# Performance work log

Hardware: AMD Instinct MI355X
Metric: run time of the kernel (lower is better)

The kernel has to match this reference:

```python
import jax, jax.numpy as jnp
import numpy as np

B, N, C = 8, 2048, 256
NGRP = 4          # n oscillator dims per group
RANK = 16         # A_rank
EPS = 1e-6        # solver eps
GN_EPS = 1e-5     # torch GroupNorm default eps


def setup_inputs() -> dict:
    key = jax.random.key(0)
    k0, k1, k2, k3 = jax.random.split(key, 4)
    x = jax.random.normal(k0, (B, N, C), jnp.float32)
    y = jax.random.normal(k1, (B, C, N), jnp.float32)
    sc = jax.random.uniform(k2, (B, N, N), jnp.float32)
    U = 0.01 * jax.random.normal(k3, (N, RANK), jnp.float32)
    omega_param = (1.0 / np.sqrt(2)).astype(np.float32) * jnp.ones((C // 2, 1), jnp.float32)
    gn_w = jnp.ones((C,), jnp.float32)
    gn_b = jnp.zeros((C,), jnp.float32)
    gamma = jnp.float32(1.0)
    return {"x": x, "y": y, "sc": sc, "U": U, "omega_param": omega_param,
            "gn_w": gn_w, "gn_b": gn_b, "gamma": gamma, "Q": 8}


def _map_to_sphere(x):
    # normalize each group of NGRP channels to unit norm
    xv = x.reshape(B, N, C // NGRP, NGRP)
    n2 = jnp.clip(jnp.sum(xv * xv, axis=-1, keepdims=True), EPS, None)
    return (xv * jax.lax.rsqrt(n2)).reshape(B, N, C)


def _project_osc(v, x):
    # remove component of v along x within each oscillator group (tangent projection)
    xv = x.reshape(B, N, C // NGRP, NGRP)
    vv = v.reshape(B, N, C // NGRP, NGRP)
    sim = jnp.sum(xv * vv, axis=-1, keepdims=True)
    return (vv - sim * xv).reshape(B, N, C)


def _group_norm(y, w, b):
    # y: [B, C, N]; num_groups = C // NGRP, NGRP channels per group
    G = C // NGRP
    yv = y.reshape(B, G, NGRP * N)
    mu = jnp.mean(yv, axis=-1, keepdims=True)
    var = jnp.mean((yv - mu) ** 2, axis=-1, keepdims=True)
    yn = ((yv - mu) * jax.lax.rsqrt(var + GN_EPS)).reshape(B, C, N)
    return yn * w[None, :, None] + b[None, :, None]


def _omega_term(x, omega_param):
    # pairwise rotation: (x0, x1) -> (omg*x1, -omg*x0), omg = |omega_param| per pair
    xp = x.reshape(B, N, C // 2, 2)
    omg = jnp.abs(omega_param).reshape(1, 1, C // 2)  # norm over trailing dim of size 1
    out = jnp.stack([omg * xp[..., 1], -omg * xp[..., 0]], axis=-1)
    return out.reshape(B, N, C)


def _kuramoto(x, y, sc, U, omega_param, gn_w, gn_b, gamma, Q):
    rho = 1.0
    # y: [B, C, N] -> GroupNorm -> [B, N, C] -> sphere
    y = _group_norm(y, gn_w, gn_b)
    y = _map_to_sphere(jnp.transpose(y, (0, 2, 1)))
    # x: [B, N, C] (N != C so no transpose in original)
    x = _map_to_sphere(x)
    # coupling matrix K = sym(W) * sigmoid(U U^T)  (normalize_K=False, w_scale=1)
    Wsym = 0.5 * (sc + jnp.transpose(sc, (0, 2, 1)))
    A = jax.nn.sigmoid(U @ U.T)          # [N, N]
    K = Wsym * A[None, :, :]             # [B, N, N]

    def step(xc, _):
        coupling = jnp.einsum('bnm,bmc->bnc', K, xc)
        force = coupling + y
        om = _omega_term(xc, omega_param)
        dxdt = om + rho * _project_osc(force, xc)
        xn = _map_to_sphere(xc + gamma * dxdt)
        return xn, xn

    _, xs = jax.lax.scan(step, x, None, length=Q)
    return xs  # [Q, B, N, C]


def reference(x, y, sc, U, omega_param, gn_w, gn_b, gamma, Q):
    return _kuramoto(x, y, sc, U, omega_param, gn_w, gn_b, gamma, Q)
```

## Files before the change

### kernel.cpp

```cpp
#include <hip/hip_runtime.h>
#include <hip/hip_bf16.h>

#define BB 8
#define NN 2048
#define CC 256
#define GG 64
#define QQ 8

typedef unsigned short u16;
typedef __attribute__((ext_vector_type(8))) short bf16x8;
typedef __attribute__((ext_vector_type(4))) float f32x4;

static __device__ __forceinline__ float b2f(u16 u) {
  union { unsigned int i; float f; } cv; cv.i = ((unsigned int)u) << 16; return cv.f;
}
static __device__ __forceinline__ u16 f2b(float f) {
  union { __hip_bfloat16 h; u16 u; } cv; cv.h = __float2bfloat16(f); return cv.u;
}
static __device__ __forceinline__ float ldin(const void* p, size_t i, bool f32) {
  return f32 ? ((const float*)p)[i] : b2f(((const u16*)p)[i]);
}
static __device__ __forceinline__ float4 ldin4(const void* p, size_t i, bool f32) {
  if (f32) return *(const float4*)((const float*)p + i);
  ushort4 u = *(const ushort4*)((const u16*)p + i);
  return make_float4(b2f(u.x), b2f(u.y), b2f(u.z), b2f(u.w));
}
static __device__ __forceinline__ void gload16(const void* g, void* l) {
  __builtin_amdgcn_global_load_lds(
      (const __attribute__((address_space(1))) void*)g,
      (__attribute__((address_space(3))) void*)l, 16, 0, 0);
}

__global__ __launch_bounds__(256) void detect_kernel(const u16* __restrict__ sc,
                                                     int* __restrict__ flag)
{
  __shared__ int sh;
  if (threadIdx.x == 0) sh = 0;
  __syncthreads();
  int cnt = 0;
  for (int i = threadIdx.x; i < 2048; i += 256) {
    u16 w = sc[2 * i];
    int e = (w >> 7) & 0xFF;
    if (e >= 100 && e <= 130) cnt++;
  }
  atomicAdd(&sh, cnt);
  __syncthreads();
  if (threadIdx.x == 0) *flag = (sh < 1024) ? 1 : 0;
}

__global__ __launch_bounds__(256) void build_k_kernel(
    const void* __restrict__ sc, const void* __restrict__ U,
    u16* __restrict__ Khi, u16* __restrict__ Klo,
    const int* __restrict__ flagp, int b0)
{
  const int i0 = blockIdx.y * 32;
  const int j0 = blockIdx.x * 32;
  if (j0 < i0) return;
  const bool f32 = (*flagp != 0);
  const int bl = blockIdx.z;
  const int b  = b0 + bl;
  const int tx = threadIdx.x;
  const int ty = threadIdx.y;
  const int t  = ty * 32 + tx;
  const int rr = t >> 3;
  const int cq = t & 7;

  __shared__ float Ui[32][17];
  __shared__ float Uj[32][17];
  __shared__ float As[32][33];
  __shared__ float t1[32][33];
  __shared__ float t2[32][33];

  for (int s = t; s < 512; s += 256) {
    int r2 = s >> 4, kk = s & 15;
    Ui[r2][kk] = ldin(U, (size_t)(i0 + r2) * 16 + kk, f32);
    Uj[r2][kk] = ldin(U, (size_t)(j0 + r2) * 16 + kk, f32);
  }
  const size_t scb = (size_t)b * NN * NN;
  float4 va = ldin4(sc, scb + (size_t)(i0 + rr) * NN + j0 + 4 * cq, f32);
  float4 vb = ldin4(sc, scb + (size_t)(j0 + rr) * NN + i0 + 4 * cq, f32);
  __syncthreads();
  for (int ii = ty; ii < 32; ii += 8) {
    float dot = 0.f;
    #pragma unroll
    for (int k = 0; k < 16; k++) dot += Ui[ii][k] * Uj[tx][k];
    As[ii][tx] = 1.0f / (1.0f + expf(-dot));
  }
  t1[rr][4*cq+0] = va.x; t1[rr][4*cq+1] = va.y;
  t1[rr][4*cq+2] = va.z; t1[rr][4*cq+3] = va.w;
  t2[rr][4*cq+0] = vb.x; t2[rr][4*cq+1] = vb.y;
  t2[rr][4*cq+2] = vb.z; t2[rr][4*cq+3] = vb.w;
  __syncthreads();

  const size_t kfb = (size_t)bl * NN * NN;
  ushort4 h4, l4;
  #pragma unroll
  for (int k = 0; k < 4; k++) {
    int col = 4 * cq + k;
    float kv = 0.5f * (t1[rr][col] + t2[col][rr]) * As[rr][col];
    u16 h = f2b(kv);
    ((u16*)&h4)[k] = h;
    ((u16*)&l4)[k] = f2b(kv - b2f(h));
  }
  size_t o = kfb + (size_t)(i0 + rr) * NN + j0 + 4 * cq;
  *(ushort4*)(Khi + o) = h4;
  *(ushort4*)(Klo + o) = l4;
  if (i0 != j0) {
    #pragma unroll
    for (int k = 0; k < 4; k++) {
      int col = 4 * cq + k;
      float kv = 0.5f * (t2[rr][col] + t1[col][rr]) * As[col][rr];
      u16 h = f2b(kv);
      ((u16*)&h4)[k] = h;
      ((u16*)&l4)[k] = f2b(kv - b2f(h));
    }
    size_t o2 = kfb + (size_t)(j0 + rr) * NN + i0 + 4 * cq;
    *(ushort4*)(Khi + o2) = h4;
    *(ushort4*)(Klo + o2) = l4;
  }
}

__global__ __launch_bounds__(256) void gn_stats_kernel(
    const void* __restrict__ y, float* __restrict__ murs,
    const int* __restrict__ flagp)
{
  const bool f32 = (*flagp != 0);
  const int bg = blockIdx.x;
  float s = 0.f, ss = 0.f;
  if (f32) {
    const float* base = (const float*)y + (size_t)bg * 4 * NN;
    for (int i = threadIdx.x; i < 2048; i += 256) {
      float4 v = *(const float4*)(base + (size_t)i * 4);
      s  += v.x + v.y + v.z + v.w;
      ss += v.x*v.x + v.y*v.y + v.z*v.z + v.w*v.w;
    }
  } else {
    const u16* base = (const u16*)y + (size_t)bg * 4 * NN;
    for (int i = threadIdx.x; i < 2048; i += 256) {
      ushort4 v = *(const ushort4*)(base + (size_t)i * 4);
      float f0 = b2f(v.x), f1 = b2f(v.y), f2 = b2f(v.z), f3 = b2f(v.w);
      s  += f0 + f1 + f2 + f3;
      ss += f0*f0 + f1*f1 + f2*f2 + f3*f3;
    }
  }
  #pragma unroll
  for (int off = 32; off > 0; off >>= 1) {
    s  += __shfl_down(s, off, 64);
    ss += __shfl_down(ss, off, 64);
  }
  __shared__ float sh[8];
  const int w = threadIdx.x >> 6, ln = threadIdx.x & 63;
  if (ln == 0) { sh[w * 2] = s; sh[w * 2 + 1] = ss; }
  __syncthreads();
  if (threadIdx.x == 0) {
    float S  = sh[0] + sh[2] + sh[4] + sh[6];
    float SS = sh[1] + sh[3] + sh[5] + sh[7];
    float mu  = S / 8192.0f;
    float var = SS / 8192.0f - mu * mu;
    murs[bg * 2]     = mu;
    murs[bg * 2 + 1] = 1.0f / sqrtf(fmaxf(var, 0.f) + 1e-5f);
  }
}

__global__ __launch_bounds__(256) void y_tf_kernel(
    const void* __restrict__ y, const float* __restrict__ murs,
    const void* __restrict__ gw, const void* __restrict__ gb,
    float* __restrict__ yt, const int* __restrict__ flagp)
{
  const bool f32 = (*flagp != 0);
  const int b = blockIdx.y;
  const int n = blockIdx.x * 64 + threadIdx.x;
  for (int g = threadIdx.y; g < GG; g += 4) {
    float mu = murs[(b * GG + g) * 2];
    float rs = murs[(b * GG + g) * 2 + 1];
    float v[4];
    #pragma unroll
    for (int k = 0; k < 4; k++) {
      int c = 4 * g + k;
      float val = (ldin(y, ((size_t)b * CC + c) * NN + n, f32) - mu) * rs;
      v[k] = val * ldin(gw, c, f32) + ldin(gb, c, f32);
    }
    float n2 = v[0]*v[0] + v[1]*v[1] + v[2]*v[2] + v[3]*v[3];
    float scl = 1.0f / sqrtf(fmaxf(n2, 1e-6f));
    float4 o; o.x = v[0]*scl; o.y = v[1]*scl; o.z = v[2]*scl; o.w = v[3]*scl;
    *(float4*)(yt + ((size_t)b * NN + n) * CC + 4 * g) = o;
  }
}

__global__ __launch_bounds__(256) void x_init_kernel(
    const void* __restrict__ x, u16* __restrict__ xTh, u16* __restrict__ xTl,
    const int* __restrict__ flagp)
{
  const bool f32 = (*flagp != 0);
  const int b = blockIdx.y;
  const int n = blockIdx.x * 64 + threadIdx.x;
  for (int g = threadIdx.y; g < GG; g += 4) {
    size_t idx = ((size_t)b * NN + n) * CC + 4 * g;
    float v[4];
    if (f32) {
      float4 u4 = *(const float4*)((const float*)x + idx);
      v[0] = u4.x; v[1] = u4.y; v[2] = u4.z; v[3] = u4.w;
    } else {
      ushort4 u = *(const ushort4*)((const u16*)x + idx);
      v[0] = b2f(u.x); v[1] = b2f(u.y); v[2] = b2f(u.z); v[3] = b2f(u.w);
    }
    float n2 = v[0]*v[0] + v[1]*v[1] + v[2]*v[2] + v[3]*v[3];
    float scl = 1.0f / sqrtf(fmaxf(n2, 1e-6f));
    size_t xb = ((size_t)b * CC + 4 * g) * NN + n;
    #pragma unroll
    for (int k = 0; k < 4; k++) {
      float xv = v[k] * scl;
      u16 h = f2b(xv);
      xTh[xb + (size_t)k * NN] = h;
      xTl[xb + (size_t)k * NN] = f2b(xv - b2f(h));
    }
  }
}

template<int NFR, int NFC>
static __device__ __forceinline__ void fused_step_epilogue(
    f32x4 (&acc)[NFR][NFC], int b, int rb, int cb, int l15, int lk,
    const u16* __restrict__ xhc, const u16* __restrict__ xlc,
    u16* __restrict__ xhn, u16* __restrict__ xln,
    const float* __restrict__ yt, const void* __restrict__ omega,
    const void* __restrict__ gamma, void* __restrict__ outbase, size_t qoff,
    bool f32)
{
  const float gm = ldin(gamma, 0, f32);
  #pragma unroll
  for (int fr = 0; fr < NFR; fr++) {
    const int rbase = rb + fr * 16 + lk * 4;
    #pragma unroll
    for (int fc = 0; fc < NFC; fc++) {
      const int c = cb + fc * 16 + l15;
      const size_t xoff = ((size_t)b * CC + c) * NN + rbase;
      ushort4 xh4 = *(const ushort4*)(xhc + xoff);
      ushort4 xl4 = *(const ushort4*)(xlc + xoff);
      float xcv[4] = { b2f(xh4.x) + b2f(xl4.x), b2f(xh4.y) + b2f(xl4.y),
                       b2f(xh4.z) + b2f(xl4.z), b2f(xh4.w) + b2f(xl4.w) };
      float om   = fabsf(ldin(omega, c >> 1, f32));
      float omsg = (c & 1) ? -om : om;
      float xn[4];
      #pragma unroll
      for (int r = 0; r < 4; r++) {
        const int n = rbase + r;
        float f = acc[fr][fc][r] + yt[((size_t)b * NN + n) * CC + c];
        float s = xcv[r] * f;
        s += __shfl_xor(s, 1);
        s += __shfl_xor(s, 2);
        float xp = __shfl_xor(xcv[r], 1);
        float d  = omsg * xp + (f - s * xcv[r]);
        float v  = xcv[r] + gm * d;
        float n2 = v * v;
        n2 += __shfl_xor(n2, 1);
        n2 += __shfl_xor(n2, 2);
        float scl = 1.0f / sqrtf(fmaxf(n2, 1e-6f));
        xn[r] = v * scl;
        const size_t oidx = qoff + ((size_t)b * NN + n) * CC + c;
        if (f32) __builtin_nontemporal_store(xn[r], (float*)outbase + oidx);
        else     __builtin_nontemporal_store(f2b(xn[r]), (u16*)outbase + oidx);
      }
      ushort4 nh, nl;
      #pragma unroll
      for (int r = 0; r < 4; r++) {
        u16 h = f2b(xn[r]);
        ((u16*)&nh)[r] = h;
        ((u16*)&nl)[r] = f2b(xn[r] - b2f(h));
      }
      *(ushort4*)(xhn + xoff) = nh;
      *(ushort4*)(xln + xoff) = nl;
    }
  }
}

__global__ __launch_bounds__(512, 2) void gemm_fused_p10(
    const u16* __restrict__ Khi, const u16* __restrict__ Klo,
    const u16* __restrict__ xhc, const u16* __restrict__ xlc,
    u16* __restrict__ xhn, u16* __restrict__ xln,
    const float* __restrict__ yt, const void* __restrict__ omega,
    const void* __restrict__ gamma, void* __restrict__ outbase, size_t qoff,
    const int* __restrict__ flagp)
{
  const int flat = blockIdx.x + 2 * blockIdx.y + 32 * blockIdx.z;
  const int swz  = (flat & 7) * 32 + (flat >> 3);
  const int bx = swz & 1;
  const int by = (swz >> 1) & 15;
  const int b  = swz >> 5;
  const int m0 = by * 128;
  const int c0 = bx * 128;

  __shared__ char lds[2][65536];

  const int t    = threadIdx.x;
  const int lane = t & 63;
  const int wid  = t >> 6;
  const int ng   = wid >> 2;
  const int wr   = (wid >> 1) & 1;
  const int wc   = wid & 1;

  const u16* Ah = Khi + (size_t)b * NN * NN;
  const u16* Al = Klo + (size_t)b * NN * NN;
  const u16* Bh = xhc + (size_t)b * CC * NN;
  const u16* Bl = xlc + (size_t)b * CC * NN;

  const int tr   = t >> 3;
  const int phys = (t & 7) ^ (tr & 7);
  const size_t aoff = (size_t)(m0 + tr) * NN + phys * 8;
  const size_t boff = (size_t)(c0 + tr) * NN + phys * 8;
  const int dst = wid * 1024;

  f32x4 acc[4][2];
  const f32x4 zero4 = {0.f, 0.f, 0.f, 0.f};
  #pragma unroll
  for (int i = 0; i < 4; i++)
    #pragma unroll
    for (int j = 0; j < 2; j++) acc[i][j] = zero4;

  auto stage = [&](int bufi, int kt) {
    char* base = &lds[bufi][0];
    const int k0 = kt * 64;
    #pragma unroll
    for (int i = 0; i < 2; i++) {
      gload16(Ah + aoff + (size_t)i * (64 * NN) + k0, base +         i * 8192 + dst);
      gload16(Al + aoff + (size_t)i * (64 * NN) + k0, base + 16384 + i * 8192 + dst);
      gload16(Bh + boff + (size_t)i * (64 * NN) + k0, base + 32768 + i * 8192 + dst);
      gload16(Bl + boff + (size_t)i * (64 * NN) + k0, base + 49152 + i * 8192 + dst);
    }
  };

  const int l15 = lane & 15;
  const int lk  = lane >> 4;

  auto compute = [&](int bufi) {
    const char* base = &lds[bufi][0];
    #pragma unroll
    for (int ks = 0; ks < 2; ks++) {
      const int cl = ks * 4 + lk;
      bf16x8 fah[4], fal[4], fbh[2], fbl[2];
      #pragma unroll
      for (int fr = 0; fr < 4; fr++) {
        int r   = wr * 64 + fr * 16 + l15;
        int off = r * 128 + ((cl ^ (r & 7)) << 4);
        fah[fr] = *(const bf16x8*)(base + off);
        fal[fr] = *(const bf16x8*)(base + 16384 + off);
      }
      #pragma unroll
      for (int fc = 0; fc < 2; fc++) {
        int r   = ng * 64 + wc * 32 + fc * 16 + l15;
        int off = r * 128 + ((cl ^ (r & 7)) << 4);
        fbh[fc] = *(const bf16x8*)(base + 32768 + off);
        fbl[fc] = *(const bf16x8*)(base + 49152 + off);
      }
      #pragma unroll
      for (int fr = 0; fr < 4; fr++)
        #pragma unroll
        for (int fc = 0; fc < 2; fc++) {
          acc[fr][fc] = __builtin_amdgcn_mfma_f32_16x16x32_bf16(
              fah[fr], fbh[fc], acc[fr][fc], 0, 0, 0);
          acc[fr][fc] = __builtin_amdgcn_mfma_f32_16x16x32_bf16(
              fah[fr], fbl[fc], acc[fr][fc], 0, 0, 0);
          acc[fr][fc] = __builtin_amdgcn_mfma_f32_16x16x32_bf16(
              fal[fr], fbh[fc], acc[fr][fc], 0, 0, 0);
        }
    }
  };

  stage(0, 0);
  __syncthreads();
  int buf = 0;
  for (int kt = 0; kt < NN / 64; kt++) {
    if (kt + 1 < NN / 64) stage(buf ^ 1, kt + 1);
    compute(buf);
    __syncthreads();
    buf ^= 1;
  }

  fused_step_epilogue<4, 2>(acc, b, m0 + wr * 64, c0 + ng * 64 + wc * 32,
                            l15, lk, xhc, xlc, xhn, xln, yt, omega, gamma,
                            outbase, qoff, (*flagp != 0));
}

__global__ __launch_bounds__(256, 2) void gemm_fused_db(
    const u16* __restrict__ Khi, const u16* __restrict__ Klo,
    const u16* __restrict__ xhc, const u16* __restrict__ xlc,
    u16* __restrict__ xhn, u16* __restrict__ xln,
    const float* __restrict__ yt, const void* __restrict__ omega,
    const void* __restrict__ gamma, void* __restrict__ outbase, size_t qoff,
    const int* __restrict__ flagp, int grp)
{
  const int flat = blockIdx.x + 4 * blockIdx.y + 128 * blockIdx.z;
  const int swz  = (flat & 7) * 64 + (flat >> 3);
  const int bx = swz & 3;
  const int by = (swz >> 2) & 31;
  const int bl = swz >> 7;
  const int b  = grp * 4 + bl;
  const int m0 = by * 64;
  const int c0 = bx * 64;

  __shared__ char lds[2][32768];

  const int t    = threadIdx.x;
  const int lane = t & 63;
  const int wid  = t >> 6;
  const int wr   = wid >> 1;
  const int wc   = wid & 1;

  const u16* Ah = Khi + (size_t)bl * NN * NN;
  const u16* Al = Klo + (size_t)bl * NN * NN;
  const u16* Bh = xhc + (size_t)b * CC * NN;
  const u16* Bl = xlc + (size_t)b * CC * NN;

  const int tr   = t >> 3;
  const int phys = (t & 7) ^ (tr & 7);
  const size_t aoff = (size_t)(m0 + tr) * NN + phys * 8;
  const size_t boff = (size_t)(c0 + tr) * NN + phys * 8;
  const int dst = wid * 1024;

  f32x4 acc[2][2];
  const f32x4 zero4 = {0.f, 0.f, 0.f, 0.f};
  #pragma unroll
  for (int i = 0; i < 2; i++)
    #pragma unroll
    for (int j = 0; j < 2; j++) acc[i][j] = zero4;

  auto stage = [&](int bufi, int kt) {
    char* base = &lds[bufi][0];
    const int k0 = kt * 64;
    #pragma unroll
    for (int i = 0; i < 2; i++) {
      gload16(Ah + aoff + (size_t)i * (32 * NN) + k0, base +         i * 4096 + dst);
      gload16(Al + aoff + (size_t)i * (32 * NN) + k0, base +  8192 + i * 4096 + dst);
      gload16(Bh + boff + (size_t)i * (32 * NN) + k0, base + 16384 + i * 4096 + dst);
      gload16(Bl + boff + (size_t)i * (32 * NN) + k0, base + 24576 + i * 4096 + dst);
    }
  };

  const int l15 = lane & 15;
  const int lk  = lane >> 4;

  auto compute = [&](int bufi) {
    const char* base = &lds[bufi][0];
    #pragma unroll
    for (int ks = 0; ks < 2; ks++) {
      const int cl = ks * 4 + lk;
      bf16x8 fah[2], fal[2], fbh[2], fbl[2];
      #pragma unroll
      for (int fr = 0; fr < 2; fr++) {
        int r   = wr * 32 + fr * 16 + l15;
        int off = r * 128 + ((cl ^ (r & 7)) << 4);
        fah[fr] = *(const bf16x8*)(base + off);
        fal[fr] = *(const bf16x8*)(base + 8192 + off);
      }
      #pragma unroll
      for (int fc = 0; fc < 2; fc++) {
        int r   = wc * 32 + fc * 16 + l15;
        int off = r * 128 + ((cl ^ (r & 7)) << 4);
        fbh[fc] = *(const bf16x8*)(base + 16384 + off);
        fbl[fc] = *(const bf16x8*)(base + 24576 + off);
      }
      #pragma unroll
      for (int fr = 0; fr < 2; fr++)
        #pragma unroll
        for (int fc = 0; fc < 2; fc++) {
          acc[fr][fc] = __builtin_amdgcn_mfma_f32_16x16x32_bf16(
              fah[fr], fbh[fc], acc[fr][fc], 0, 0, 0);
          acc[fr][fc] = __builtin_amdgcn_mfma_f32_16x16x32_bf16(
              fah[fr], fbl[fc], acc[fr][fc], 0, 0, 0);
          acc[fr][fc] = __builtin_amdgcn_mfma_f32_16x16x32_bf16(
              fal[fr], fbh[fc], acc[fr][fc], 0, 0, 0);
        }
    }
  };

  stage(0, 0);
  __syncthreads();
  int buf = 0;
  for (int kt = 0; kt < NN / 64; kt++) {
    if (kt + 1 < NN / 64) stage(buf ^ 1, kt + 1);
    compute(buf);
    __syncthreads();
    buf ^= 1;
  }

  fused_step_epilogue<2, 2>(acc, b, m0 + wr * 32, c0 + wc * 32,
                            l15, lk, xhc, xlc, xhn, xln, yt, omega, gamma,
                            outbase, qoff, (*flagp != 0));
}

extern "C" void kernel_launch(void* const* d_in, const int* in_sizes, int n_in,
                              void* d_out, int out_size, void* d_ws, size_t ws_size,
                              hipStream_t stream) {
  const void* x     = d_in[0];
  const void* y     = d_in[1];
  const void* sc    = d_in[2];
  const void* U     = d_in[3];
  const void* omega = d_in[4];
  const void* gw    = d_in[5];
  const void* gb    = d_in[6];
  const void* gamma = d_in[7];
  char* ws = (char*)d_ws;

  const size_t BNC = (size_t)BB * NN * CC;
  const bool big = ws_size >= 184600000ull;

  if (big) {
    u16*   Khi  = (u16*)(ws);
    u16*   Klo  = (u16*)(ws + 67108864);
    float* yt   = (float*)(ws + 134217728);
    u16*   xAh  = (u16*)(ws + 150994944);
    u16*   xAl  = (u16*)(ws + 159383552);
    u16*   xBh  = (u16*)(ws + 167772160);
    u16*   xBl  = (u16*)(ws + 176160768);
    float* murs = (float*)(ws + 184549376);
    int*   flag = (int*)  (ws + 184553472);
    u16* xh[2] = { xAh, xBh };
    u16* xl[2] = { xAl, xBl };

    detect_kernel<<<dim3(1), dim3(256), 0, stream>>>((const u16*)sc, flag);
    gn_stats_kernel<<<dim3(512), dim3(256), 0, stream>>>(y, murs, flag);
    y_tf_kernel<<<dim3(32, 8), dim3(64, 4), 0, stream>>>(y, murs, gw, gb, yt, flag);
    x_init_kernel<<<dim3(32, 8), dim3(64, 4), 0, stream>>>(x, xAh, xAl, flag);
    build_k_kernel<<<dim3(64, 64, 8), dim3(32, 8), 0, stream>>>(
        sc, U, Khi, Klo, flag, 0);
    for (int q = 0; q < QQ; q++) {
      const int cur = q & 1, nxt = cur ^ 1;
      gemm_fused_p10<<<dim3(2, 16, 8), dim3(512), 0, stream>>>(
          Khi, Klo, xh[cur], xl[cur], xh[nxt], xl[nxt],
          yt, omega, gamma, d_out, (size_t)q * BNC, flag);
    }
  } else {
    u16*   Khi  = (u16*)(ws);
    u16*   Klo  = (u16*)(ws + 33554432);
    float* yt   = (float*)(ws + 67108864);
    u16*   xAh  = (u16*)(ws + 83886080);
    u16*   xAl  = (u16*)(ws + 92274688);
    u16*   xBh  = (u16*)(ws + 100663296);
    u16*   xBl  = (u16*)(ws + 109051904);
    float* murs = (float*)(ws + 117440512);
    int*   flag = (int*)  (ws + 117444608);
    u16* xh[2] = { xAh, xBh };
    u16* xl[2] = { xAl, xBl };

    detect_kernel<<<dim3(1), dim3(256), 0, stream>>>((const u16*)sc, flag);
    gn_stats_kernel<<<dim3(512), dim3(256), 0, stream>>>(y, murs, flag);
    y_tf_kernel<<<dim3(32, 8), dim3(64, 4), 0, stream>>>(y, murs, gw, gb, yt, flag);
    x_init_kernel<<<dim3(32, 8), dim3(64, 4), 0, stream>>>(x, xAh, xAl, flag);
    for (int grp = 0; grp < 2; grp++) {
      build_k_kernel<<<dim3(64, 64, 4), dim3(32, 8), 0, stream>>>(
          sc, U, Khi, Klo, flag, grp * 4);
      for (int q = 0; q < QQ; q++) {
        const int cur = q & 1, nxt = cur ^ 1;
        gemm_fused_db<<<dim3(4, 32, 4), dim3(256), 0, stream>>>(
            Khi, Klo, xh[cur], xl[cur], xh[nxt], xl[nxt],
            yt, omega, gamma, d_out, (size_t)q * BNC, flag, grp);
      }
    }
  }
}
```

Measured before the change: 854.4 us.

## Replace double-buffered LDS staging with single buffer to raise occupancy

The GEMM kernel's LDS is cut from two 64 KB buffers to one, and the loop changes from prefetching the next K tile during compute to load, sync, compute, sync. This halves shared memory per block so more blocks fit per CU (launch bounds ask for 2). In exchange, the overlap of global loads with MFMA work inside a block is lost, and the per-iteration barriers rise from one to two.

```diff
diff --git a/kernel.cpp b/kernel.cpp
--- a/kernel.cpp
+++ b/kernel.cpp
@@ -273,7 +273,7 @@
   }
 }
 
-__global__ __launch_bounds__(512, 2) void gemm_fused_p10(
+__global__ __launch_bounds__(512, 2) void gemm_fused_r12(
     const u16* __restrict__ Khi, const u16* __restrict__ Klo,
     const u16* __restrict__ xhc, const u16* __restrict__ xlc,
     u16* __restrict__ xhn, u16* __restrict__ xln,
@@ -289,7 +289,7 @@
   const int m0 = by * 128;
   const int c0 = bx * 128;
 
-  __shared__ char lds[2][65536];
+  __shared__ char lds[65536];
 
   const int t    = threadIdx.x;
   const int lane = t & 63;
@@ -316,23 +316,21 @@
     #pragma unroll
     for (int j = 0; j < 2; j++) acc[i][j] = zero4;
 
-  auto stage = [&](int bufi, int kt) {
-    char* base = &lds[bufi][0];
+  auto stage = [&](int kt) {
     const int k0 = kt * 64;
     #pragma unroll
     for (int i = 0; i < 2; i++) {
-      gload16(Ah + aoff + (size_t)i * (64 * NN) + k0, base +         i * 8192 + dst);
-      gload16(Al + aoff + (size_t)i * (64 * NN) + k0, base + 16384 + i * 8192 + dst);
-      gload16(Bh + boff + (size_t)i * (64 * NN) + k0, base + 32768 + i * 8192 + dst);
-      gload16(Bl + boff + (size_t)i * (64 * NN) + k0, base + 49152 + i * 8192 + dst);
+      gload16(Ah + aoff + (size_t)i * (64 * NN) + k0, lds +         i * 8192 + dst);
+      gload16(Al + aoff + (size_t)i * (64 * NN) + k0, lds + 16384 + i * 8192 + dst);
+      gload16(Bh + boff + (size_t)i * (64 * NN) + k0, lds + 32768 + i * 8192 + dst);
+      gload16(Bl + boff + (size_t)i * (64 * NN) + k0, lds + 49152 + i * 8192 + dst);
     }
   };
 
   const int l15 = lane & 15;
   const int lk  = lane >> 4;
 
-  auto compute = [&](int bufi) {
-    const char* base = &lds[bufi][0];
+  auto compute = [&]() {
     #pragma unroll
     for (int ks = 0; ks < 2; ks++) {
       const int cl = ks * 4 + lk;
@@ -341,15 +339,15 @@
       for (int fr = 0; fr < 4; fr++) {
         int r   = wr * 64 + fr * 16 + l15;
         int off = r * 128 + ((cl ^ (r & 7)) << 4);
-        fah[fr] = *(const bf16x8*)(base + off);
-        fal[fr] = *(const bf16x8*)(base + 16384 + off);
+        fah[fr] = *(const bf16x8*)(lds + off);
+        fal[fr] = *(const bf16x8*)(lds + 16384 + off);
       }
       #pragma unroll
       for (int fc = 0; fc < 2; fc++) {
         int r   = ng * 64 + wc * 32 + fc * 16 + l15;
         int off = r * 128 + ((cl ^ (r & 7)) << 4);
-        fbh[fc] = *(const bf16x8*)(base + 32768 + off);
-        fbl[fc] = *(const bf16x8*)(base + 49152 + off);
+        fbh[fc] = *(const bf16x8*)(lds + 32768 + off);
+        fbl[fc] = *(const bf16x8*)(lds + 49152 + off);
       }
       #pragma unroll
       for (int fr = 0; fr < 4; fr++)
@@ -365,14 +363,11 @@
     }
   };
 
-  stage(0, 0);
-  __syncthreads();
-  int buf = 0;
   for (int kt = 0; kt < NN / 64; kt++) {
-    if (kt + 1 < NN / 64) stage(buf ^ 1, kt + 1);
-    compute(buf);
+    stage(kt);
     __syncthreads();
-    buf ^= 1;
+    compute();
+    __syncthreads();
   }
 
   fused_step_epilogue<4, 2>(acc, b, m0 + wr * 64, c0 + ng * 64 + wc * 32,
@@ -524,7 +519,7 @@
         sc, U, Khi, Klo, flag, 0);
     for (int q = 0; q < QQ; q++) {
       const int cur = q & 1, nxt = cur ^ 1;
-      gemm_fused_p10<<<dim3(2, 16, 8), dim3(512), 0, stream>>>(
+      gemm_fused_r12<<<dim3(2, 16, 8), dim3(512), 0, stream>>>(
           Khi, Klo, xh[cur], xl[cur], xh[nxt], xl[nxt],
           yt, omega, gamma, d_out, (size_t)q * BNC, flag);
     }
```

Measured after the change: 986.8 us. +15.5%, slower.
